# Kernel tuning notes

Hardware: AMD Instinct MI355X
Metric: run time of the kernel (lower is better)

The kernel has to match this reference:

```python
import jax, jax.numpy as jnp
import numpy as np

BS, L, D, H, NL, ITEM_NUM = 128, 64, 512, 8, 2, 100000
NEG_INF = -10000.0


def _ln(x):
    m = jnp.mean(x, axis=-1, keepdims=True)
    v = jnp.var(x, axis=-1, keepdims=True)
    return (x - m) * jax.lax.rsqrt(v + 1e-5)


def _user_encoder(input_embs, log_mask, pos_emb, qkv_w, out_w, ffn_w1, ffn_w2):
    # SASRec-style causal transformer encoder (post-LN blocks)
    B, S, d = input_embs.shape
    dh = d // H
    x = _ln(input_embs + pos_emb[None, :, :])
    pad = (log_mask != 0)                                  # [B,S]
    causal = jnp.tril(jnp.ones((S, S), dtype=bool))
    attn_ok = causal[None, :, :] & pad[:, None, :]         # [B,S,S]
    bias = jnp.where(attn_ok, 0.0, NEG_INF)[:, None, :, :]  # [B,1,S,S]
    for l in range(NL):
        qkv = x @ qkv_w[l]                                 # [B,S,3d]
        q, k, v = jnp.split(qkv, 3, axis=-1)
        q = q.reshape(B, S, H, dh).transpose(0, 2, 1, 3)
        k = k.reshape(B, S, H, dh).transpose(0, 2, 1, 3)
        v = v.reshape(B, S, H, dh).transpose(0, 2, 1, 3)
        scores = jnp.einsum('bhqd,bhkd->bhqk', q, k) / jnp.sqrt(jnp.asarray(dh, x.dtype)) + bias
        attn = jax.nn.softmax(scores, axis=-1)
        o = jnp.einsum('bhqk,bhkd->bhqd', attn, v).transpose(0, 2, 1, 3).reshape(B, S, d)
        x = _ln(x + o @ out_w[l])
        h = jax.nn.gelu(x @ ffn_w1[l])
        x = _ln(x + h @ ffn_w2[l])
    return x


def setup_inputs() -> dict:
    key = jax.random.key(0)
    ks = jax.random.split(key, 9)
    sample_items_id = jax.random.randint(ks[0], (BS, L + 1), 0, ITEM_NUM + 1)
    log_mask = jax.random.randint(ks[1], (BS, L), 0, 2).astype(jnp.float32)
    emb_table = (jax.random.normal(ks[2], (ITEM_NUM + 1, D), jnp.float32) * 0.02).at[0].set(0.0)
    pos_emb = jax.random.normal(ks[3], (L, D), jnp.float32) * 0.02
    qkv_w = jax.random.normal(ks[4], (NL, D, 3 * D), jnp.float32) * (D ** -0.5)
    out_w = jax.random.normal(ks[5], (NL, D, D), jnp.float32) * (D ** -0.5)
    ffn_w1 = jax.random.normal(ks[6], (NL, D, 4 * D), jnp.float32) * (D ** -0.5)
    ffn_w2 = jax.random.normal(ks[7], (NL, 4 * D, D), jnp.float32) * ((4 * D) ** -0.5)
    pop_prob = jax.random.uniform(ks[8], (ITEM_NUM + 1,), jnp.float32, 1e-6, 1.0)
    return dict(sample_items_id=sample_items_id, log_mask=log_mask, emb_table=emb_table,
                pos_emb=pos_emb, qkv_w=qkv_w, out_w=out_w, ffn_w1=ffn_w1, ffn_w2=ffn_w2,
                pop_prob=pop_prob)


def reference(sample_items_id, log_mask, emb_table, pos_emb, qkv_w, out_w, ffn_w1, ffn_w2, pop_prob):
    bs, l = log_mask.shape
    N = bs * (l + 1)
    items_flat = sample_items_id.reshape(-1)                        # [N]
    debias = jnp.log(pop_prob[items_flat])                          # [N]
    score_embs = emb_table[items_flat]                              # [N, D]
    input_embs = score_embs.reshape(bs, l + 1, -1)
    prec = _user_encoder(input_embs[:, :-1, :], log_mask, pos_emb, qkv_w, out_w, ffn_w1, ffn_w2)
    prec = prec.reshape(bs * l, -1)                                 # [bs*L, D]
    logits = prec @ score_embs.T - debias[None, :]                  # [bs*L, N]
    # padding-column mask (concat(log_mask, ones) == 0)
    pad_cols = jnp.concatenate([log_mask, jnp.ones((bs, 1), log_mask.dtype)], axis=1).reshape(-1) == 0
    logits = jnp.where(pad_cols[None, :], NEG_INF, logits)
    logits = logits.reshape(bs, l, N)
    # in-batch dedup mask: column k masked for batch i if item k appears in batch i's items
    id_list = sample_items_id.reshape(bs, l + 1)
    member = (items_flat[None, :, None] == id_list[:, None, :]).any(-1)   # [bs, N]
    target_col = jnp.arange(bs)[:, None] * (l + 1) + jnp.arange(1, l + 1)[None, :]  # [bs, L]
    is_target = jnp.arange(N)[None, None, :] == target_col[:, :, None]    # [bs, L, N]
    dedup = member[:, None, :] & ~is_target
    logits = jnp.where(dedup, NEG_INF, logits).reshape(bs * l, N)
    labels = target_col.reshape(-1)                                 # [bs*L]
    logp = jax.nn.log_softmax(logits, axis=-1)
    nll = -jnp.take_along_axis(logp, labels[:, None], axis=1)[:, 0]
    valid = (log_mask.reshape(-1) != 0).astype(logits.dtype)
    return (nll * valid).sum() / valid.sum()
```

## Files before the change

kernel.cpp:

```cpp
#include <hip/hip_runtime.h>
#include <hip/hip_bf16.h>
#include <cstdint>
#include <cstddef>

#define NEG_INF -10000.0f

constexpr int BSZ  = 128;
constexpr int SEQ  = 64;
constexpr int DIM  = 512;
constexpr int HEADS = 8;
constexpr int NLAYER = 2;
constexpr int NCOL = BSZ * (SEQ + 1);
constexpr int NCOLP = 8448;
constexpr int NROW = BSZ * SEQ;
constexpr int NSTRIP = NCOLP / 64;
constexpr float CMAX = 40.0f;

typedef __attribute__((ext_vector_type(8))) short bf16x8;
typedef __attribute__((ext_vector_type(4))) float f32x4;

__device__ __forceinline__ void async_copy16(const void* g, void* l) {
    __builtin_amdgcn_global_load_lds(
        (const __attribute__((address_space(1))) void*)g,
        (__attribute__((address_space(3))) void*)l, 16, 0, 0);
}

__device__ __forceinline__ float b2f(uint16_t u) {
    return __builtin_bit_cast(float, (uint32_t)u << 16);
}
__device__ __forceinline__ uint16_t f2b(float f) {
    __hip_bfloat16 h = __float2bfloat16(f);
    return __builtin_bit_cast(uint16_t, h);
}

__device__ __forceinline__ float gelu_f(float v) {
    float u = 0.7978845608028654f * (v + 0.044715f * v * v * v);
    return 0.5f * v * (1.0f + tanhf(u));
}

__device__ __forceinline__ void swizzle_rc(int id, int& ry, int& cx) {
    ry = (id & 7) * 8 + ((id >> 3) & 7);
    cx = id >> 6;
}

#define BAR() __builtin_amdgcn_s_barrier()
#define LGKM0() asm volatile("s_waitcnt lgkmcnt(0)" ::: "memory")
#define VMCNT(n) asm volatile("s_waitcnt vmcnt(" #n ")" ::: "memory")

__global__ __launch_bounds__(256) void gather_posln_kernel(
    const int* __restrict__ ids, const float* __restrict__ table,
    const float* __restrict__ pop, const float* __restrict__ pos,
    __hip_bfloat16* __restrict__ sebf, float* __restrict__ debias,
    __hip_bfloat16* __restrict__ xb) {
    const int w = threadIdx.x >> 6, lane = threadIdx.x & 63;
    const int k = blockIdx.x * 4 + w;
    const int b = k / 65, s = k - b * 65;
    const int id = ids[k];
    const float* src = table + (size_t)id * DIM + lane * 8;
    float4 u0 = *(const float4*)src;
    float4 u1 = *(const float4*)(src + 4);
    float v[8] = {u0.x, u0.y, u0.z, u0.w, u1.x, u1.y, u1.z, u1.w};
    bf16x8 se;
    #pragma unroll
    for (int j = 0; j < 8; j++) se[j] = (short)f2b(v[j]);
    *(bf16x8*)((uint16_t*)sebf + (size_t)k * DIM + lane * 8) = se;
    if (lane == 0) debias[k] = logf(pop[id]);
    if (s < 64) {
        const float* pp = pos + (size_t)s * DIM + lane * 8;
        float4 p0 = *(const float4*)pp;
        float4 p1 = *(const float4*)(pp + 4);
        float t[8] = {v[0] + p0.x, v[1] + p0.y, v[2] + p0.z, v[3] + p0.w,
                      v[4] + p1.x, v[5] + p1.y, v[6] + p1.z, v[7] + p1.w};
        float sum = 0.f, sq = 0.f;
        #pragma unroll
        for (int j = 0; j < 8; j++) { sum += t[j]; sq += t[j] * t[j]; }
        #pragma unroll
        for (int off = 32; off > 0; off >>= 1) {
            sum += __shfl_xor(sum, off, 64);
            sq  += __shfl_xor(sq,  off, 64);
        }
        const float mean = sum * (1.0f / 512.0f);
        const float var  = sq * (1.0f / 512.0f) - mean * mean;
        const float rs = rsqrtf(var + 1e-5f);
        bf16x8 o;
        #pragma unroll
        for (int j = 0; j < 8; j++) o[j] = (short)f2b((t[j] - mean) * rs);
        *(bf16x8*)((uint16_t*)xb + (size_t)(b * 64 + s) * DIM + lane * 8) = o;
    }
}

__global__ __launch_bounds__(256) void mask_kernel(
    const int* __restrict__ ids, const float* __restrict__ log_mask,
    uint8_t* __restrict__ colmask, uint8_t* __restrict__ padcol) {
    const int bi = blockIdx.x >> 3, seg = blockIdx.x & 7;
    __shared__ int sid[65];
    if (threadIdx.x < 65) sid[threadIdx.x] = ids[bi * 65 + threadIdx.x];
    __syncthreads();
    const int kend = (seg + 1) * (NCOLP / 8);
    for (int k = seg * (NCOLP / 8) + threadIdx.x; k < kend; k += 256) {
        uint8_t cmv, pcv;
        if (k < NCOL) {
            const int id = ids[k];
            bool mem = false;
            #pragma unroll
            for (int j = 0; j < 65; j++) mem |= (sid[j] == id);
            const int i2 = k / 65, jj = k - i2 * 65;
            const bool pc = (jj < 64) && (log_mask[i2 * 64 + jj] == 0.0f);
            cmv = (mem || pc) ? 1 : 0;
            pcv = pc ? 1 : 0;
        } else { cmv = 1; pcv = 1; }
        colmask[(size_t)bi * NCOLP + k] = cmv;
        if (bi == 0) padcol[k] = pcv;
    }
}

__global__ __launch_bounds__(256) void transpose_bf16_kernel(
    const float* __restrict__ W, __hip_bfloat16* __restrict__ WT, int K, int N) {
    __shared__ float tile[32][33];
    const size_t loff = (size_t)blockIdx.z * K * N;
    const int nt = blockIdx.x * 32, kt = blockIdx.y * 32;
    const int c = threadIdx.x & 31, r = threadIdx.x >> 5;
    #pragma unroll
    for (int p = 0; p < 4; p++)
        tile[p * 8 + r][c] = W[loff + (size_t)(kt + p * 8 + r) * N + nt + c];
    __syncthreads();
    #pragma unroll
    for (int p = 0; p < 4; p++)
        WT[loff + (size_t)(nt + p * 8 + r) * K + kt + c] = __float2bfloat16(tile[c][p * 8 + r]);
}

__global__ __launch_bounds__(256) void resid_ln_kernel(
    __hip_bfloat16* __restrict__ xb, const __hip_bfloat16* __restrict__ y) {
    const int w = threadIdx.x >> 6, lane = threadIdx.x & 63;
    const int row = blockIdx.x * 4 + w;
    uint16_t* xp = (uint16_t*)xb + (size_t)row * DIM + lane * 8;
    const uint16_t* yp = (const uint16_t*)y + (size_t)row * DIM + lane * 8;
    bf16x8 xv = *(const bf16x8*)xp;
    bf16x8 yv = *(const bf16x8*)yp;
    float t[8];
    float sum = 0.f, sq = 0.f;
    #pragma unroll
    for (int j = 0; j < 8; j++) {
        t[j] = b2f((uint16_t)xv[j]) + b2f((uint16_t)yv[j]);
        sum += t[j]; sq += t[j] * t[j];
    }
    #pragma unroll
    for (int off = 32; off > 0; off >>= 1) {
        sum += __shfl_xor(sum, off, 64);
        sq  += __shfl_xor(sq,  off, 64);
    }
    const float mean = sum * (1.0f / 512.0f);
    const float var  = sq * (1.0f / 512.0f) - mean * mean;
    const float rs = rsqrtf(var + 1e-5f);
    bf16x8 o;
    #pragma unroll
    for (int j = 0; j < 8; j++) o[j] = (short)f2b((t[j] - mean) * rs);
    *(bf16x8*)xp = o;
}

template<int TN, bool GELU>
__global__ __launch_bounds__(256) void gemm_bt_kernel(
    const __hip_bfloat16* __restrict__ A, const __hip_bfloat16* __restrict__ Bt,
    __hip_bfloat16* __restrict__ C, int N, int K) {
    __shared__ uint16_t As[2][128][32];
    __shared__ uint16_t Bs[2][TN][32];
    const int tid = threadIdx.x, w = tid >> 6, lane = tid & 63;
    const int quad = lane >> 4, l15 = lane & 15;
    constexpr int AI = (TN == 128) ? 4 : 2;
    const int wr = (TN == 128) ? (w >> 1) : w;
    const int wc = (TN == 128) ? (w & 1) : 0;
    const int rowbase = wr * (AI * 16);
    int ry, cx;
    swizzle_rc(blockIdx.x, ry, cx);
    const int row0 = ry * 128, col0 = cx * TN;
    const uint16_t* Ag = (const uint16_t*)A;
    const uint16_t* Bg = (const uint16_t*)Bt;
    const int sr = lane >> 2, sc = (lane & 3) * 8;
    f32x4 acc[AI][4];
    #pragma unroll
    for (int i = 0; i < AI; i++)
        #pragma unroll
        for (int j = 0; j < 4; j++) acc[i][j] = {0.f, 0.f, 0.f, 0.f};

    for (int k0 = 0; k0 < K; k0 += 64) {
        #pragma unroll
        for (int h = 0; h < 2; h++) {
            #pragma unroll
            for (int i = 0; i < 2; i++) {
                const int rb = w * 32 + i * 16;
                async_copy16(Ag + (size_t)(row0 + rb + sr) * K + k0 + h * 32 + sc, &As[h][rb][0]);
            }
            if (TN == 128) {
                #pragma unroll
                for (int i = 0; i < 2; i++) {
                    const int rb = w * 32 + i * 16;
                    async_copy16(Bg + (size_t)(col0 + rb + sr) * K + k0 + h * 32 + sc, &Bs[h][rb][0]);
                }
            } else {
                const int rb = w * 16;
                async_copy16(Bg + (size_t)(col0 + rb + sr) * K + k0 + h * 32 + sc, &Bs[h][rb][0]);
            }
        }
        __syncthreads();
        #pragma unroll
        for (int h = 0; h < 2; h++) {
            bf16x8 af[AI], bfr[4];
            #pragma unroll
            for (int i = 0; i < AI; i++)
                af[i] = *(const bf16x8*)&As[h][rowbase + i * 16 + l15][quad * 8];
            #pragma unroll
            for (int j = 0; j < 4; j++)
                bfr[j] = *(const bf16x8*)&Bs[h][wc * 64 + j * 16 + l15][quad * 8];
            #pragma unroll
            for (int i = 0; i < AI; i++)
                #pragma unroll
                for (int j = 0; j < 4; j++)
                    acc[i][j] = __builtin_amdgcn_mfma_f32_16x16x32_bf16(af[i], bfr[j], acc[i][j], 0, 0, 0);
        }
        __syncthreads();
    }
    #pragma unroll
    for (int i = 0; i < AI; i++) {
        #pragma unroll
        for (int r = 0; r < 4; r++) {
            const int row = row0 + rowbase + i * 16 + quad * 4 + r;
            #pragma unroll
            for (int j = 0; j < 4; j++) {
                const int col = col0 + wc * 64 + j * 16 + l15;
                float v = acc[i][j][r];
                if (GELU) v = gelu_f(v);
                C[(size_t)row * N + col] = __float2bfloat16(v);
            }
        }
    }
}

__global__ __launch_bounds__(256) void attn_mfma_kernel(
    const __hip_bfloat16* __restrict__ qkv, const float* __restrict__ log_mask,
    __hip_bfloat16* __restrict__ obuf) {
    constexpr int QS = 72;
    constexpr int VS32 = 36;
    __shared__ uint16_t Qs[64 * QS];
    __shared__ uint16_t Ks_[64 * QS];
    __shared__ uint16_t Ps[64 * QS];
    __shared__ uint32_t Vt32[64 * VS32];
    __shared__ float mask_s[64];
    const int b = blockIdx.x >> 3, h = blockIdx.x & 7;
    const int tid = threadIdx.x, w = tid >> 6, lane = tid & 63;
    const int quad = lane >> 4, l15 = lane & 15;
    const uint16_t* qg = (const uint16_t*)qkv;

    if (tid < 64) mask_s[tid] = log_mask[b * 64 + tid];
    #pragma unroll
    for (int it = 0; it < 2; it++) {
        const int idx = it * 256 + tid;
        const int s = idx >> 3, c = (idx & 7) * 8;
        const size_t gbase = (size_t)(b * 64 + s) * 1536 + h * 64 + c;
        *(bf16x8*)&Qs[s * QS + c]  = *(const bf16x8*)&qg[gbase];
        *(bf16x8*)&Ks_[s * QS + c] = *(const bf16x8*)&qg[gbase + 512];
    }
    {
        const int sp = tid >> 3;
        const int c = (tid & 7) * 8;
        const size_t gbase = (size_t)(b * 64 + sp * 2) * 1536 + 1024 + h * 64 + c;
        bf16x8 v0 = *(const bf16x8*)&qg[gbase];
        bf16x8 v1 = *(const bf16x8*)&qg[gbase + 1536];
        #pragma unroll
        for (int jj = 0; jj < 8; jj++)
            Vt32[(c + jj) * VS32 + sp] =
                (uint32_t)(uint16_t)v0[jj] | ((uint32_t)(uint16_t)v1[jj] << 16);
    }
    __syncthreads();

    f32x4 sacc[4];
    #pragma unroll
    for (int j = 0; j < 4; j++) sacc[j] = {0.f, 0.f, 0.f, 0.f};
    #pragma unroll
    for (int k0 = 0; k0 < 2; k0++) {
        bf16x8 aq = *(const bf16x8*)&Qs[(w * 16 + l15) * QS + k0 * 32 + quad * 8];
        #pragma unroll
        for (int j = 0; j < 4; j++) {
            bf16x8 bk = *(const bf16x8*)&Ks_[(j * 16 + l15) * QS + k0 * 32 + quad * 8];
            sacc[j] = __builtin_amdgcn_mfma_f32_16x16x32_bf16(aq, bk, sacc[j], 0, 0, 0);
        }
    }
    #pragma unroll
    for (int r = 0; r < 4; r++) {
        const int q = w * 16 + quad * 4 + r;
        float vals[4];
        float vmax = -3.0e38f;
        #pragma unroll
        for (int j = 0; j < 4; j++) {
            const int col = j * 16 + l15;
            const bool ok = (col <= q) && (mask_s[col] != 0.0f);
            float v = sacc[j][r] * 0.125f + (ok ? 0.0f : NEG_INF);
            vals[j] = v;
            vmax = fmaxf(vmax, v);
        }
        #pragma unroll
        for (int off = 1; off < 16; off <<= 1) vmax = fmaxf(vmax, __shfl_xor(vmax, off, 64));
        float e[4], s = 0.f;
        #pragma unroll
        for (int j = 0; j < 4; j++) { e[j] = __expf(vals[j] - vmax); s += e[j]; }
        #pragma unroll
        for (int off = 1; off < 16; off <<= 1) s += __shfl_xor(s, off, 64);
        const float inv = 1.0f / s;
        #pragma unroll
        for (int j = 0; j < 4; j++)
            Ps[q * QS + j * 16 + l15] = f2b(e[j] * inv);
    }
    __syncthreads();

    f32x4 oacc[4];
    #pragma unroll
    for (int j = 0; j < 4; j++) oacc[j] = {0.f, 0.f, 0.f, 0.f};
    #pragma unroll
    for (int k0 = 0; k0 < 2; k0++) {
        bf16x8 ap = *(const bf16x8*)&Ps[(w * 16 + l15) * QS + k0 * 32 + quad * 8];
        #pragma unroll
        for (int j = 0; j < 4; j++) {
            bf16x8 bv = *(const bf16x8*)&Vt32[(j * 16 + l15) * VS32 + k0 * 16 + quad * 4];
            oacc[j] = __builtin_amdgcn_mfma_f32_16x16x32_bf16(ap, bv, oacc[j], 0, 0, 0);
        }
    }
    #pragma unroll
    for (int r = 0; r < 4; r++) {
        const int q = w * 16 + quad * 4 + r;
        #pragma unroll
        for (int j = 0; j < 4; j++) {
            const int d = j * 16 + l15;
            obuf[(size_t)(b * 64 + q) * 512 + h * 64 + d] = __float2bfloat16(oacc[j][r]);
        }
    }
}

template<int EPI>
__global__ __launch_bounds__(512) void gemm256_kernel(
    const __hip_bfloat16* __restrict__ A, const __hip_bfloat16* __restrict__ Bt,
    __hip_bfloat16* __restrict__ C, int N, int K,
    const float* __restrict__ debias, const uint8_t* __restrict__ colmask,
    float* __restrict__ partials) {
    __shared__ uint16_t SA[2][2][128 * 64];
    __shared__ uint16_t SB[2][2][128 * 64];
    __shared__ float dc_s[256];
    __shared__ uint8_t cm_s[4][256];

    const int tid = threadIdx.x;
    const int w = tid >> 6, lane = tid & 63;
    const int quad = lane >> 4, l15 = lane & 15;
    const int wr = w >> 2, wc = w & 3;

    const int nwg = gridDim.x;
    const int xid = (blockIdx.x & 7) * (nwg >> 3) + (blockIdx.x >> 3);
    const int ry = xid & 31, cx = xid >> 5;
    const int row0 = ry * 256, col0 = cx * 256;

    const uint16_t* Ag = (const uint16_t*)A;
    const uint16_t* Bg = (const uint16_t*)Bt;

    if (EPI == 2) {
        if (tid < 256) dc_s[tid] = debias[col0 + tid] + CMAX;
        #pragma unroll
        for (int j = 0; j < 2; j++) {
            const int e = j * 512 + tid;
            cm_s[e >> 8][e & 255] =
                colmask[(size_t)((row0 >> 6) + (e >> 8)) * NCOLP + col0 + (e & 255)];
        }
    }

    const int tb0 = w << 6, tb1 = 512 + (w << 6);
    const uint16_t* gA[2][2];
    const uint16_t* gB[2][2];
    #pragma unroll
    for (int j = 0; j < 2; j++) {
        const int t = j * 512 + (w << 6) + lane;
        const int r = t >> 3;
        const int s = (t & 7) ^ (r & 7);
        #pragma unroll
        for (int h = 0; h < 2; h++) {
            gA[h][j] = Ag + (size_t)(row0 + h * 128 + r) * K + s * 8;
            gB[h][j] = Bg + (size_t)(col0 + h * 128 + r) * K + s * 8;
        }
    }

    #define STAGE_A(tile, half, k0) do { \
        async_copy16(gA[half][0] + (k0), &SA[tile][half][tb0 * 8]); \
        async_copy16(gA[half][1] + (k0), &SA[tile][half][tb1 * 8]); } while (0)
    #define STAGE_B(tile, half, k0) do { \
        async_copy16(gB[half][0] + (k0), &SB[tile][half][tb0 * 8]); \
        async_copy16(gB[half][1] + (k0), &SB[tile][half][tb1 * 8]); } while (0)

    auto fragA = [&](int tile, int m, int kk) -> bf16x8 {
        return *(const bf16x8*)&SA[tile][wr]
            [((m * 16 + l15) << 6) + ((((kk << 2) + quad) ^ (l15 & 7)) << 3)];
    };
    auto fragB = [&](int tile, int n, int kk) -> bf16x8 {
        return *(const bf16x8*)&SB[tile][wc >> 1]
            [(((wc & 1) * 64 + n * 16 + l15) << 6) + ((((kk << 2) + quad) ^ (l15 & 7)) << 3)];
    };

    f32x4 acc[8][4];
    #pragma unroll
    for (int m = 0; m < 8; m++)
        #pragma unroll
        for (int n = 0; n < 4; n++) acc[m][n] = {0.f, 0.f, 0.f, 0.f};

    STAGE_A(0, 0, 0); STAGE_A(0, 1, 0);
    STAGE_B(0, 0, 0); STAGE_B(0, 1, 0);
    STAGE_A(1, 0, 64); STAGE_B(1, 0, 64);
    VMCNT(4);
    BAR();

    const int niters = K >> 7;
    bf16x8 af[4][2], bA[2][2], bB[2][2];
    for (int it = 0; it < niters; ++it) {
        const bool st = (it + 1 < niters);
        const int kc = it << 7;
        const int kn = kc + 128;

        #pragma unroll
        for (int m = 0; m < 4; m++) { af[m][0] = fragA(0, m, 0); af[m][1] = fragA(0, m, 1); }
        #pragma unroll
        for (int n = 0; n < 2; n++) { bA[n][0] = fragB(0, n, 0); bA[n][1] = fragB(0, n, 1); }
        STAGE_A(1, 1, kc + 64);
        BAR(); LGKM0();
        __builtin_amdgcn_s_setprio(1);
        #pragma unroll
        for (int m = 0; m < 4; m++)
            #pragma unroll
            for (int n = 0; n < 2; n++) {
                acc[m][n] = __builtin_amdgcn_mfma_f32_16x16x32_bf16(af[m][0], bA[n][0], acc[m][n], 0, 0, 0);
                acc[m][n] = __builtin_amdgcn_mfma_f32_16x16x32_bf16(af[m][1], bA[n][1], acc[m][n], 0, 0, 0);
            }
        __builtin_amdgcn_s_setprio(0);
        BAR();

        #pragma unroll
        for (int n = 0; n < 2; n++) { bB[n][0] = fragB(0, n + 2, 0); bB[n][1] = fragB(0, n + 2, 1); }
        STAGE_B(1, 1, kc + 64);
        BAR(); LGKM0();
        __builtin_amdgcn_s_setprio(1);
        #pragma unroll
        for (int m = 0; m < 4; m++)
            #pragma unroll
            for (int n = 0; n < 2; n++) {
                acc[m][n + 2] = __builtin_amdgcn_mfma_f32_16x16x32_bf16(af[m][0], bB[n][0], acc[m][n + 2], 0, 0, 0);
                acc[m][n + 2] = __builtin_amdgcn_mfma_f32_16x16x32_bf16(af[m][1], bB[n][1], acc[m][n + 2], 0, 0, 0);
            }
        __builtin_amdgcn_s_setprio(0);
        BAR();

        #pragma unroll
        for (int m = 0; m < 4; m++) { af[m][0] = fragA(0, m + 4, 0); af[m][1] = fragA(0, m + 4, 1); }
        if (st) STAGE_B(0, 0, kn);
        BAR(); LGKM0();
        __builtin_amdgcn_s_setprio(1);
        #pragma unroll
        for (int m = 0; m < 4; m++)
            #pragma unroll
            for (int n = 0; n < 2; n++) {
                acc[m + 4][n + 2] = __builtin_amdgcn_mfma_f32_16x16x32_bf16(af[m][0], bB[n][0], acc[m + 4][n + 2], 0, 0, 0);
                acc[m + 4][n + 2] = __builtin_amdgcn_mfma_f32_16x16x32_bf16(af[m][1], bB[n][1], acc[m + 4][n + 2], 0, 0, 0);
            }
        __builtin_amdgcn_s_setprio(0);
        BAR();

        if (st) STAGE_A(0, 0, kn);
        __builtin_amdgcn_s_setprio(1);
        #pragma unroll
        for (int m = 0; m < 4; m++)
            #pragma unroll
            for (int n = 0; n < 2; n++) {
                acc[m + 4][n] = __builtin_amdgcn_mfma_f32_16x16x32_bf16(af[m][0], bA[n][0], acc[m + 4][n], 0, 0, 0);
                acc[m + 4][n] = __builtin_amdgcn_mfma_f32_16x16x32_bf16(af[m][1], bA[n][1], acc[m + 4][n], 0, 0, 0);
            }
        __builtin_amdgcn_s_setprio(0);
        if (st) { VMCNT(4); } else { VMCNT(0); }
        BAR();

        #pragma unroll
        for (int m = 0; m < 4; m++) { af[m][0] = fragA(1, m, 0); af[m][1] = fragA(1, m, 1); }
        #pragma unroll
        for (int n = 0; n < 2; n++) { bA[n][0] = fragB(1, n, 0); bA[n][1] = fragB(1, n, 1); }
        if (st) STAGE_A(0, 1, kn);
        BAR(); LGKM0();
        __builtin_amdgcn_s_setprio(1);
        #pragma unroll
        for (int m = 0; m < 4; m++)
            #pragma unroll
            for (int n = 0; n < 2; n++) {
                acc[m][n] = __builtin_amdgcn_mfma_f32_16x16x32_bf16(af[m][0], bA[n][0], acc[m][n], 0, 0, 0);
                acc[m][n] = __builtin_amdgcn_mfma_f32_16x16x32_bf16(af[m][1], bA[n][1], acc[m][n], 0, 0, 0);
            }
        __builtin_amdgcn_s_setprio(0);
        BAR();

        #pragma unroll
        for (int n = 0; n < 2; n++) { bB[n][0] = fragB(1, n + 2, 0); bB[n][1] = fragB(1, n + 2, 1); }
        if (st) STAGE_B(0, 1, kn);
        BAR(); LGKM0();
        __builtin_amdgcn_s_setprio(1);
        #pragma unroll
        for (int m = 0; m < 4; m++)
            #pragma unroll
            for (int n = 0; n < 2; n++) {
                acc[m][n + 2] = __builtin_amdgcn_mfma_f32_16x16x32_bf16(af[m][0], bB[n][0], acc[m][n + 2], 0, 0, 0);
                acc[m][n + 2] = __builtin_amdgcn_mfma_f32_16x16x32_bf16(af[m][1], bB[n][1], acc[m][n + 2], 0, 0, 0);
            }
        __builtin_amdgcn_s_setprio(0);
        BAR();

        #pragma unroll
        for (int m = 0; m < 4; m++) { af[m][0] = fragA(1, m + 4, 0); af[m][1] = fragA(1, m + 4, 1); }
        if (st) STAGE_B(1, 0, kn + 64);
        BAR(); LGKM0();
        __builtin_amdgcn_s_setprio(1);
        #pragma unroll
        for (int m = 0; m < 4; m++)
            #pragma unroll
            for (int n = 0; n < 2; n++) {
                acc[m + 4][n + 2] = __builtin_amdgcn_mfma_f32_16x16x32_bf16(af[m][0], bB[n][0], acc[m + 4][n + 2], 0, 0, 0);
                acc[m + 4][n + 2] = __builtin_amdgcn_mfma_f32_16x16x32_bf16(af[m][1], bB[n][1], acc[m + 4][n + 2], 0, 0, 0);
            }
        __builtin_amdgcn_s_setprio(0);
        BAR();

        if (st) STAGE_A(1, 0, kn + 64);
        __builtin_amdgcn_s_setprio(1);
        #pragma unroll
        for (int m = 0; m < 4; m++)
            #pragma unroll
            for (int n = 0; n < 2; n++) {
                acc[m + 4][n] = __builtin_amdgcn_mfma_f32_16x16x32_bf16(af[m][0], bA[n][0], acc[m + 4][n], 0, 0, 0);
                acc[m + 4][n] = __builtin_amdgcn_mfma_f32_16x16x32_bf16(af[m][1], bA[n][1], acc[m + 4][n], 0, 0, 0);
            }
        __builtin_amdgcn_s_setprio(0);
        if (st) { VMCNT(4); BAR(); }
    }

    if (EPI == 2) {
        const int strip = cx * 4 + wc;
        #pragma unroll
        for (int m = 0; m < 8; m++) {
            #pragma unroll
            for (int r = 0; r < 4; r++) {
                const int lrow = wr * 128 + m * 16 + quad * 4 + r;
                const int row = row0 + lrow;
                float s = 0.f;
                #pragma unroll
                for (int n = 0; n < 4; n++) {
                    const int lcol = wc * 64 + n * 16 + l15;
                    float t = acc[m][n][r] - dc_s[lcol];
                    t = (cm_s[lrow >> 6][lcol] != 0) ? -1.0e30f : t;
                    s += __expf(t);
                }
                #pragma unroll
                for (int off = 1; off < 16; off <<= 1) s += __shfl_xor(s, off, 64);
                if (l15 == 0) partials[(size_t)row * NSTRIP + strip] = s;
            }
        }
    } else {
        #pragma unroll
        for (int m = 0; m < 8; m++) {
            #pragma unroll
            for (int r = 0; r < 4; r++) {
                const int row = row0 + wr * 128 + m * 16 + quad * 4 + r;
                #pragma unroll
                for (int n = 0; n < 4; n++) {
                    const int col = col0 + wc * 64 + n * 16 + l15;
                    float v = acc[m][n][r];
                    if (EPI == 1) v = gelu_f(v);
                    C[(size_t)row * N + col] = __float2bfloat16(v);
                }
            }
        }
    }
    #undef STAGE_A
    #undef STAGE_B
}

__global__ __launch_bounds__(256) void label_kernel(
    const __hip_bfloat16* __restrict__ xb, const __hip_bfloat16* __restrict__ sebf,
    const float* __restrict__ debias, const uint8_t* __restrict__ padcol,
    float* __restrict__ lab) {
    const int w = threadIdx.x >> 6, lane = threadIdx.x & 63;
    const int row = blockIdx.x * 4 + w;
    const int b = row >> 6, s0 = row & 63;
    const int k = b * 65 + s0 + 1;
    const uint16_t* xp = (const uint16_t*)xb + (size_t)row * DIM + lane * 8;
    const uint16_t* sp = (const uint16_t*)sebf + (size_t)k * DIM + lane * 8;
    bf16x8 xv = *(const bf16x8*)xp;
    bf16x8 sv = *(const bf16x8*)sp;
    float a = 0.f;
    #pragma unroll
    for (int j = 0; j < 8; j++) a += b2f((uint16_t)xv[j]) * b2f((uint16_t)sv[j]);
    #pragma unroll
    for (int off = 32; off > 0; off >>= 1) a += __shfl_xor(a, off, 64);
    if (lane == 0)
        lab[row] = padcol[k] ? NEG_INF : (a - debias[k]);
}

__global__ __launch_bounds__(256) void combine_kernel(
    const float* __restrict__ partials, const float* __restrict__ label_logit,
    const float* __restrict__ log_mask, float* __restrict__ bsums) {
    const int row = blockIdx.x * 256 + threadIdx.x;
    const float lab = label_logit[row];
    float Ls = __expf(lab - CMAX);
    const float4* pr = (const float4*)(partials + (size_t)row * NSTRIP);
    for (int t = 0; t < NSTRIP / 4; t++) {
        float4 v = pr[t];
        Ls += v.x + v.y + v.z + v.w;
    }
    const float lse = CMAX + logf(Ls);
    const float valid = (log_mask[row] != 0.0f) ? 1.0f : 0.0f;
    float a = (lse - lab) * valid;
    float c = valid;
    __shared__ float sa[4], sc_[4];
    #pragma unroll
    for (int off = 32; off > 0; off >>= 1) {
        a += __shfl_down(a, off, 64);
        c += __shfl_down(c, off, 64);
    }
    const int lane = threadIdx.x & 63, w = threadIdx.x >> 6;
    if (lane == 0) { sa[w] = a; sc_[w] = c; }
    __syncthreads();
    if (threadIdx.x == 0) {
        bsums[blockIdx.x * 2 + 0] = sa[0] + sa[1] + sa[2] + sa[3];
        bsums[blockIdx.x * 2 + 1] = sc_[0] + sc_[1] + sc_[2] + sc_[3];
    }
}

__global__ __launch_bounds__(64) void finalize_kernel(
    const float* __restrict__ bsums, float* __restrict__ out) {
    const int t = threadIdx.x;
    float a = 0.f, c = 0.f;
    if (t < 32) { a = bsums[2 * t]; c = bsums[2 * t + 1]; }
    #pragma unroll
    for (int off = 32; off > 0; off >>= 1) {
        a += __shfl_down(a, off, 64);
        c += __shfl_down(c, off, 64);
    }
    if (t == 0) out[0] = a / c;
}

extern "C" void kernel_launch(void* const* d_in, const int* in_sizes, int n_in,
                              void* d_out, int out_size, void* d_ws, size_t ws_size,
                              hipStream_t stream) {
    const int*   ids    = (const int*)d_in[0];
    const float* lm     = (const float*)d_in[1];
    const float* emb    = (const float*)d_in[2];
    const float* pos    = (const float*)d_in[3];
    const float* qkv_w  = (const float*)d_in[4];
    const float* out_w  = (const float*)d_in[5];
    const float* ffn1_w = (const float*)d_in[6];
    const float* ffn2_w = (const float*)d_in[7];
    const float* pop    = (const float*)d_in[8];
    float* out = (float*)d_out;

    char* p = (char*)d_ws;
    auto alloc = [&](size_t bytes) {
        char* r = p;
        p += (bytes + 255) & ~(size_t)255;
        return r;
    };
    typedef __hip_bfloat16 bf16;
    bf16*    sebf     = (bf16*)alloc((size_t)NCOLP * DIM * 2);
    float*   debias   = (float*)alloc((size_t)NCOLP * 4);
    uint8_t* padcol   = (uint8_t*)alloc(NCOLP);
    uint8_t* colmask  = (uint8_t*)alloc((size_t)BSZ * NCOLP);
    bf16*    xb       = (bf16*)alloc((size_t)NROW * DIM * 2);
    bf16*    big      = (bf16*)alloc((size_t)NROW * 2048 * 2);
    bf16*    tmp1     = (bf16*)alloc((size_t)NROW * DIM * 2);
    bf16*    tmp2     = (bf16*)alloc((size_t)NROW * DIM * 2);
    float*   partials = (float*)alloc((size_t)NROW * NSTRIP * 4);
    float*   lab      = (float*)alloc((size_t)NROW * 4);
    float*   bsums    = (float*)alloc(64 * 4);
    bf16*    qkvT     = (bf16*)alloc((size_t)NLAYER * 1536 * 512 * 2);
    bf16*    outT     = (bf16*)alloc((size_t)NLAYER * 512 * 512 * 2);
    bf16*    f1T      = (bf16*)alloc((size_t)NLAYER * 2048 * 512 * 2);
    bf16*    f2T      = (bf16*)alloc((size_t)NLAYER * 512 * 2048 * 2);

    transpose_bf16_kernel<<<dim3(1536 / 32, 512 / 32, NLAYER), 256, 0, stream>>>(
        qkv_w, qkvT, 512, 1536);
    transpose_bf16_kernel<<<dim3(512 / 32, 512 / 32, NLAYER), 256, 0, stream>>>(
        out_w, outT, 512, 512);
    transpose_bf16_kernel<<<dim3(2048 / 32, 512 / 32, NLAYER), 256, 0, stream>>>(
        ffn1_w, f1T, 512, 2048);
    transpose_bf16_kernel<<<dim3(512 / 32, 2048 / 32, NLAYER), 256, 0, stream>>>(
        ffn2_w, f2T, 2048, 512);

    gather_posln_kernel<<<NCOL / 4, 256, 0, stream>>>(ids, emb, pop, pos, sebf, debias, xb);
    mask_kernel<<<BSZ * 8, 256, 0, stream>>>(ids, lm, colmask, padcol);

    for (int l = 0; l < NLAYER; l++) {
        gemm256_kernel<0><<<32 * (1536 / 256), 512, 0, stream>>>(
            xb, qkvT + (size_t)l * 1536 * 512, big, 1536, 512, nullptr, nullptr, nullptr);
        attn_mfma_kernel<<<BSZ * HEADS, 256, 0, stream>>>(big, lm, tmp1);
        gemm_bt_kernel<64, false><<<(512 / 64) * 64, 256, 0, stream>>>(
            tmp1, outT + (size_t)l * 512 * 512, tmp2, 512, 512);
        resid_ln_kernel<<<NROW / 4, 256, 0, stream>>>(xb, tmp2);
        gemm256_kernel<1><<<32 * (2048 / 256), 512, 0, stream>>>(
            xb, f1T + (size_t)l * 2048 * 512, big, 2048, 512, nullptr, nullptr, nullptr);
        gemm_bt_kernel<64, false><<<(512 / 64) * 64, 256, 0, stream>>>(
            big, f2T + (size_t)l * 512 * 2048, tmp2, 512, 2048);
        resid_ln_kernel<<<NROW / 4, 256, 0, stream>>>(xb, tmp2);
    }

    label_kernel<<<NROW / 4, 256, 0, stream>>>(xb, sebf, debias, padcol, lab);
    gemm256_kernel<2><<<32 * (NCOLP / 256), 512, 0, stream>>>(
        xb, sebf, nullptr, NCOLP, 512, debias, colmask, partials);
    combine_kernel<<<NROW / 256, 256, 0, stream>>>(partials, lab, lm, bsums);
    finalize_kernel<<<1, 64, 0, stream>>>(bsums, out);
}
```

Before: 655.9 us.

## Use exp2 with pre-scaled operands and switch encoder GEMMs to 128-wide tiles

Moves the log2(e) scaling into the final-layer LayerNorm output and into a precomputed debias array. The logits GEMM epilogue can then call the raw v_exp_f32 instruction directly, without a multiply per element. GELU and the attention softmax also use exp2/rcp forms in place of tanhf/__expf. The QKV and FFN1 GEMMs move from the 256-tile 512-thread kernel to the 128x128 gemm_bt kernel, which changes tiling and occupancy. It adds an extra scaled activation buffer, and scaling the activations before the bf16 rounding changes that rounding slightly.

```diff
diff --git a/kernel.cpp b/kernel.cpp
--- a/kernel.cpp
+++ b/kernel.cpp
@@ -15,6 +15,7 @@
 constexpr int NROW = BSZ * SEQ;
 constexpr int NSTRIP = NCOLP / 64;
 constexpr float CMAX = 40.0f;
+constexpr float LOG2E = 1.4426950408889634f;
 
 typedef __attribute__((ext_vector_type(8))) short bf16x8;
 typedef __attribute__((ext_vector_type(4))) float f32x4;
@@ -33,9 +34,15 @@
     return __builtin_bit_cast(uint16_t, h);
 }
 
+__device__ __forceinline__ float fexp2(float x) {
+    float r; asm("v_exp_f32 %0, %1" : "=v"(r) : "v"(x)); return r;
+}
+
 __device__ __forceinline__ float gelu_f(float v) {
     float u = 0.7978845608028654f * (v + 0.044715f * v * v * v);
-    return 0.5f * v * (1.0f + tanhf(u));
+    float t2 = fexp2(u * (2.0f * LOG2E));
+    float th = 1.0f - 2.0f * __builtin_amdgcn_rcpf(t2 + 1.0f);
+    return 0.5f * v * (1.0f + th);
 }
 
 __device__ __forceinline__ void swizzle_rc(int id, int& ry, int& cx) {
@@ -51,7 +58,7 @@
     const int* __restrict__ ids, const float* __restrict__ table,
     const float* __restrict__ pop, const float* __restrict__ pos,
     __hip_bfloat16* __restrict__ sebf, float* __restrict__ debias,
-    __hip_bfloat16* __restrict__ xb) {
+    float* __restrict__ deb2, __hip_bfloat16* __restrict__ xb) {
     const int w = threadIdx.x >> 6, lane = threadIdx.x & 63;
     const int k = blockIdx.x * 4 + w;
     const int b = k / 65, s = k - b * 65;
@@ -64,7 +71,11 @@
     #pragma unroll
     for (int j = 0; j < 8; j++) se[j] = (short)f2b(v[j]);
     *(bf16x8*)((uint16_t*)sebf + (size_t)k * DIM + lane * 8) = se;
-    if (lane == 0) debias[k] = logf(pop[id]);
+    if (lane == 0) {
+        const float lp = logf(pop[id]);
+        debias[k] = lp;
+        deb2[k] = (lp + CMAX) * LOG2E;
+    }
     if (s < 64) {
         const float* pp = pos + (size_t)s * DIM + lane * 8;
         float4 p0 = *(const float4*)pp;
@@ -129,8 +140,10 @@
         WT[loff + (size_t)(nt + p * 8 + r) * K + kt + c] = __float2bfloat16(tile[c][p * 8 + r]);
 }
 
+template<bool SCALED>
 __global__ __launch_bounds__(256) void resid_ln_kernel(
-    __hip_bfloat16* __restrict__ xb, const __hip_bfloat16* __restrict__ y) {
+    __hip_bfloat16* __restrict__ xb, const __hip_bfloat16* __restrict__ y,
+    __hip_bfloat16* __restrict__ xs) {
     const int w = threadIdx.x >> 6, lane = threadIdx.x & 63;
     const int row = blockIdx.x * 4 + w;
     uint16_t* xp = (uint16_t*)xb + (size_t)row * DIM + lane * 8;
@@ -156,6 +169,12 @@
     #pragma unroll
     for (int j = 0; j < 8; j++) o[j] = (short)f2b((t[j] - mean) * rs);
     *(bf16x8*)xp = o;
+    if (SCALED) {
+        bf16x8 os;
+        #pragma unroll
+        for (int j = 0; j < 8; j++) os[j] = (short)f2b((t[j] - mean) * rs * LOG2E);
+        *(bf16x8*)((uint16_t*)xs + (size_t)row * DIM + lane * 8) = os;
+    }
 }
 
 template<int TN, bool GELU>
@@ -301,7 +320,7 @@
         for (int off = 1; off < 16; off <<= 1) vmax = fmaxf(vmax, __shfl_xor(vmax, off, 64));
         float e[4], s = 0.f;
         #pragma unroll
-        for (int j = 0; j < 4; j++) { e[j] = __expf(vals[j] - vmax); s += e[j]; }
+        for (int j = 0; j < 4; j++) { e[j] = fexp2((vals[j] - vmax) * LOG2E); s += e[j]; }
         #pragma unroll
         for (int off = 1; off < 16; off <<= 1) s += __shfl_xor(s, off, 64);
         const float inv = 1.0f / s;
@@ -334,11 +353,10 @@
     }
 }
 
-template<int EPI>
-__global__ __launch_bounds__(512) void gemm256_kernel(
+__global__ __launch_bounds__(512) void gemm256_logits_kernel(
     const __hip_bfloat16* __restrict__ A, const __hip_bfloat16* __restrict__ Bt,
-    __hip_bfloat16* __restrict__ C, int N, int K,
-    const float* __restrict__ debias, const uint8_t* __restrict__ colmask,
+    int N, int K,
+    const float* __restrict__ deb2, const uint8_t* __restrict__ colmask,
     float* __restrict__ partials) {
     __shared__ uint16_t SA[2][2][128 * 64];
     __shared__ uint16_t SB[2][2][128 * 64];
@@ -358,14 +376,12 @@
     const uint16_t* Ag = (const uint16_t*)A;
     const uint16_t* Bg = (const uint16_t*)Bt;
 
-    if (EPI == 2) {
-        if (tid < 256) dc_s[tid] = debias[col0 + tid] + CMAX;
-        #pragma unroll
-        for (int j = 0; j < 2; j++) {
-            const int e = j * 512 + tid;
-            cm_s[e >> 8][e & 255] =
-                colmask[(size_t)((row0 >> 6) + (e >> 8)) * NCOLP + col0 + (e & 255)];
-        }
+    if (tid < 256) dc_s[tid] = deb2[col0 + tid];
+    #pragma unroll
+    for (int j = 0; j < 2; j++) {
+        const int e = j * 512 + tid;
+        cm_s[e >> 8][e & 255] =
+            colmask[(size_t)((row0 >> 6) + (e >> 8)) * NCOLP + col0 + (e & 255)];
     }
 
     const int tb0 = w << 6, tb1 = 512 + (w << 6);
@@ -538,7 +554,7 @@
         if (st) { VMCNT(4); BAR(); }
     }
 
-    if (EPI == 2) {
+    {
         const int strip = cx * 4 + wc;
         #pragma unroll
         for (int m = 0; m < 8; m++) {
@@ -552,26 +568,11 @@
                     const int lcol = wc * 64 + n * 16 + l15;
                     float t = acc[m][n][r] - dc_s[lcol];
                     t = (cm_s[lrow >> 6][lcol] != 0) ? -1.0e30f : t;
-                    s += __expf(t);
+                    s += fexp2(t);
                 }
                 #pragma unroll
                 for (int off = 1; off < 16; off <<= 1) s += __shfl_xor(s, off, 64);
                 if (l15 == 0) partials[(size_t)row * NSTRIP + strip] = s;
-            }
-        }
-    } else {
-        #pragma unroll
-        for (int m = 0; m < 8; m++) {
-            #pragma unroll
-            for (int r = 0; r < 4; r++) {
-                const int row = row0 + wr * 128 + m * 16 + quad * 4 + r;
-                #pragma unroll
-                for (int n = 0; n < 4; n++) {
-                    const int col = col0 + wc * 64 + n * 16 + l15;
-                    float v = acc[m][n][r];
-                    if (EPI == 1) v = gelu_f(v);
-                    C[(size_t)row * N + col] = __float2bfloat16(v);
-                }
             }
         }
     }
@@ -605,7 +606,7 @@
     const float* __restrict__ log_mask, float* __restrict__ bsums) {
     const int row = blockIdx.x * 256 + threadIdx.x;
     const float lab = label_logit[row];
-    float Ls = __expf(lab - CMAX);
+    float Ls = fexp2((lab - CMAX) * LOG2E);
     const float4* pr = (const float4*)(partials + (size_t)row * NSTRIP);
     for (int t = 0; t < NSTRIP / 4; t++) {
         float4 v = pr[t];
@@ -666,9 +667,11 @@
     typedef __hip_bfloat16 bf16;
     bf16*    sebf     = (bf16*)alloc((size_t)NCOLP * DIM * 2);
     float*   debias   = (float*)alloc((size_t)NCOLP * 4);
+    float*   deb2     = (float*)alloc((size_t)NCOLP * 4);
     uint8_t* padcol   = (uint8_t*)alloc(NCOLP);
     uint8_t* colmask  = (uint8_t*)alloc((size_t)BSZ * NCOLP);
     bf16*    xb       = (bf16*)alloc((size_t)NROW * DIM * 2);
+    bf16*    xbs      = (bf16*)alloc((size_t)NROW * DIM * 2);
     bf16*    big      = (bf16*)alloc((size_t)NROW * 2048 * 2);
     bf16*    tmp1     = (bf16*)alloc((size_t)NROW * DIM * 2);
     bf16*    tmp2     = (bf16*)alloc((size_t)NROW * DIM * 2);
@@ -689,26 +692,29 @@
     transpose_bf16_kernel<<<dim3(512 / 32, 2048 / 32, NLAYER), 256, 0, stream>>>(
         ffn2_w, f2T, 2048, 512);
 
-    gather_posln_kernel<<<NCOL / 4, 256, 0, stream>>>(ids, emb, pop, pos, sebf, debias, xb);
+    gather_posln_kernel<<<NCOL / 4, 256, 0, stream>>>(ids, emb, pop, pos, sebf, debias, deb2, xb);
     mask_kernel<<<BSZ * 8, 256, 0, stream>>>(ids, lm, colmask, padcol);
 
     for (int l = 0; l < NLAYER; l++) {
-        gemm256_kernel<0><<<32 * (1536 / 256), 512, 0, stream>>>(
-            xb, qkvT + (size_t)l * 1536 * 512, big, 1536, 512, nullptr, nullptr, nullptr);
+        gemm_bt_kernel<128, false><<<(1536 / 128) * 64, 256, 0, stream>>>(
+            xb, qkvT + (size_t)l * 1536 * 512, big, 1536, 512);
         attn_mfma_kernel<<<BSZ * HEADS, 256, 0, stream>>>(big, lm, tmp1);
         gemm_bt_kernel<64, false><<<(512 / 64) * 64, 256, 0, stream>>>(
             tmp1, outT + (size_t)l * 512 * 512, tmp2, 512, 512);
-        resid_ln_kernel<<<NROW / 4, 256, 0, stream>>>(xb, tmp2);
-        gemm256_kernel<1><<<32 * (2048 / 256), 512, 0, stream>>>(
-            xb, f1T + (size_t)l * 2048 * 512, big, 2048, 512, nullptr, nullptr, nullptr);
+        resid_ln_kernel<false><<<NROW / 4, 256, 0, stream>>>(xb, tmp2, nullptr);
+        gemm_bt_kernel<128, true><<<(2048 / 128) * 64, 256, 0, stream>>>(
+            xb, f1T + (size_t)l * 2048 * 512, big, 2048, 512);
         gemm_bt_kernel<64, false><<<(512 / 64) * 64, 256, 0, stream>>>(
             big, f2T + (size_t)l * 512 * 2048, tmp2, 512, 2048);
-        resid_ln_kernel<<<NROW / 4, 256, 0, stream>>>(xb, tmp2);
+        if (l == NLAYER - 1)
+            resid_ln_kernel<true><<<NROW / 4, 256, 0, stream>>>(xb, tmp2, xbs);
+        else
+            resid_ln_kernel<false><<<NROW / 4, 256, 0, stream>>>(xb, tmp2, nullptr);
     }
 
     label_kernel<<<NROW / 4, 256, 0, stream>>>(xb, sebf, debias, padcol, lab);
-    gemm256_kernel<2><<<32 * (NCOLP / 256), 512, 0, stream>>>(
-        xb, sebf, nullptr, NCOLP, 512, debias, colmask, partials);
+    gemm256_logits_kernel<<<32 * (NCOLP / 256), 512, 0, stream>>>(
+        xbs, sebf, NCOLP, 512, deb2, colmask, partials);
     combine_kernel<<<NROW / 256, 256, 0, stream>>>(partials, lab, lm, bsums);
     finalize_kernel<<<1, 64, 0, stream>>>(bsums, out);
 }
```

Result: faster. 628.1 us (-4.2%).
